# Kernel tuning notes

Hardware: AMD Instinct MI355X
Metric: run time of the kernel (lower is better)

The kernel has to match this reference:

```python
import jax, jax.numpy as jnp
import numpy as np

EPS = 1e-5
NEG_SLOPE = 0.1


def setup_inputs() -> dict:
    key = jax.random.key(0)
    ks = jax.random.split(key, 4)
    B, Cin, Cout, D, E, EMB = 2, 32, 32, 40, 3, 1
    return {
        "x": jax.random.normal(ks[0], (B, Cin, D, D, D), dtype=jnp.float32),
        "embedding": jax.random.normal(ks[1], (B, EMB), dtype=jnp.float32),
        "route_w": jax.random.normal(ks[2], (EMB, E), dtype=jnp.float32),
        "route_b": jnp.zeros((E,), dtype=jnp.float32),
        "expert_kernels": jax.random.normal(ks[3], (E, Cout, Cin, 3, 3, 3), dtype=jnp.float32) * 0.05,
        "expert_bias": jnp.zeros((E, Cout), dtype=jnp.float32),
        "gamma": jnp.ones((Cout,), dtype=jnp.float32),
        "beta": jnp.zeros((Cout,), dtype=jnp.float32),
    }


def reference(x, embedding, route_w, route_b, expert_kernels, expert_bias, gamma, beta):
    # CondConv routing: sigmoid(Linear(embedding)) -> per-sample expert weights [B, E]
    r = jax.nn.sigmoid(embedding @ route_w + route_b)
    # Per-sample combined kernel [B, O, I, 3, 3, 3] and bias [B, O]
    w = jnp.einsum('be,eoixyz->boixyz', r, expert_kernels)
    b = r @ expert_bias

    def conv_one(xi, wi):
        # xi: [Cin, D, H, W], wi: [O, I, 3, 3, 3] -> [Cout, D, H, W]
        return jax.lax.conv_general_dilated(
            xi[None], wi, window_strides=(1, 1, 1), padding='SAME',
            dimension_numbers=('NCDHW', 'OIDHW', 'NCDHW'))[0]

    y = jax.vmap(conv_one)(x, w) + b[:, :, None, None, None]  # [B, O, D, H, W]

    # BatchNorm3d (training mode: biased batch stats over B,D,H,W per channel)
    mean = jnp.mean(y, axis=(0, 2, 3, 4), keepdims=True)
    var = jnp.mean(jnp.square(y - mean), axis=(0, 2, 3, 4), keepdims=True)
    y = (y - mean) * jax.lax.rsqrt(var + EPS)
    y = y * gamma[None, :, None, None, None] + beta[None, :, None, None, None]

    # LeakyReLU(0.1)
    y = jnp.where(y >= 0, y, NEG_SLOPE * y)

    # Upsample nearest, scale_factor=2 on all 3 spatial dims
    y = jnp.repeat(jnp.repeat(jnp.repeat(y, 2, axis=2), 2, axis=3), 2, axis=4)
    return y
```

## Files before the change

kernel.cpp:

```cpp
#include <hip/hip_runtime.h>
#include <hip/hip_bf16.h>
#include <math.h>

#define BB   2
#define CIN  32
#define COUT 32
#define DM   40
#define PD   42
#define NPTS (DM*DM)
#define NVOL (DM*DM*DM)
#define EPSBN 1e-5f
#define NSLOT 64

typedef short  bf16x8  __attribute__((ext_vector_type(8)));
typedef short  bf16x4  __attribute__((ext_vector_type(4)));
typedef float  floatx4 __attribute__((ext_vector_type(4)));

#define WS_WFRAG 0
#define WS_BCOMB 27648
#define WS_SUM2  27712
#define WS_XPAD2 31808
#define WS_Y     2402624

#define REPACK_BLOCKS (PD*PD*BB)
#define NW_ELEMS  (2*2*27*64*8)
#define PREP_ELEMS (NW_ELEMS + 64 + NSLOT*64)
#define PREP_BLOCKS ((PREP_ELEMS + 255) / 256)

static __device__ __forceinline__ short f2bf(float f) {
    __hip_bfloat16 h = __float2bfloat16(f);
    return *reinterpret_cast<short*>(&h);
}
static __device__ __forceinline__ float bf2f(short s) {
    union { unsigned u; float f; } cv;
    cv.u = ((unsigned)(unsigned short)s) << 16;
    return cv.f;
}

__global__ void prep_repack_kernel(const float* __restrict__ x,
                                   const float* __restrict__ emb,
                                   const float* __restrict__ rw,
                                   const float* __restrict__ rb,
                                   const float* __restrict__ ek,
                                   const float* __restrict__ ebias,
                                   float* __restrict__ ws) {
    __shared__ __hip_bfloat16 tile[PD * 32];
    const int bid = blockIdx.x;
    const int t = threadIdx.x;
    if (bid < REPACK_BLOCKS) {
        int b  = bid / (PD * PD);
        int r  = bid % (PD * PD);
        int zp = r / PD, yp = r % PD;
        __hip_bfloat16* row = (__hip_bfloat16*)(ws + WS_XPAD2) +
                              ((((size_t)b * PD + zp) * PD + yp) * PD) * 32;
        const bool inz = (zp >= 1 && zp <= DM && yp >= 1 && yp <= DM);
        const int i  = t >> 3;
        const int xl = t & 7;
        #pragma unroll
        for (int k = 0; k < 6; ++k) {
            int xp = xl + 8 * k;
            if (xp < PD) {
                float v = 0.0f;
                if (inz && xp >= 1 && xp <= DM)
                    v = x[(size_t)(b * CIN + i) * NVOL +
                          (zp - 1) * NPTS + (yp - 1) * DM + (xp - 1)];
                tile[xp * 32 + i] = __float2bfloat16(v);
            }
        }
        __syncthreads();
        const unsigned* ts = (const unsigned*)tile;
        unsigned* rowu = (unsigned*)row;
        for (int j = t; j < PD * 32 / 2; j += 256) rowu[j] = ts[j];
        return;
    }
    int idx = (bid - REPACK_BLOCKS) * 256 + t;
    __hip_bfloat16* wfrag = (__hip_bfloat16*)(ws + WS_WFRAG);
    if (idx < NW_ELEMS) {
        int j    = idx & 7;
        int lane = (idx >> 3) & 63;
        int tap  = (idx >> 9) % 27;
        int nt   = (idx / (27 * 512)) & 1;
        int b    = idx / (2 * 27 * 512);
        int o = nt * 16 + (lane & 15);
        int i = (lane >> 4) * 8 + j;
        float e0 = emb[b];
        float w = 0.0f;
        #pragma unroll
        for (int e = 0; e < 3; ++e) {
            float r = 1.0f / (1.0f + expf(-(e0 * rw[e] + rb[e])));
            w += r * ek[((e * COUT + o) * CIN + i) * 27 + tap];
        }
        wfrag[idx] = __float2bfloat16(w);
    } else if (idx < NW_ELEMS + 64) {
        int j2 = idx - NW_ELEMS;
        int b = j2 >> 5, o = j2 & 31;
        float e0 = emb[b];
        float bv = 0.0f;
        #pragma unroll
        for (int e = 0; e < 3; ++e) {
            float r = 1.0f / (1.0f + expf(-(e0 * rw[e] + rb[e])));
            bv += r * ebias[e * COUT + o];
        }
        ws[WS_BCOMB + j2] = bv;
    } else if (idx < PREP_ELEMS) {
        ws[WS_SUM2 + (idx - NW_ELEMS - 64)] = 0.0f;
    }
}

__global__ __launch_bounds__(256, 8) void conv_mfma_kernel(
        const __hip_bfloat16* __restrict__ xp2,
        const bf16x8* __restrict__ wfrag,
        const float* __restrict__ bcomb,
        __hip_bfloat16* __restrict__ y,
        float* __restrict__ sums2) {
    const int g   = blockIdx.x & 7;
    const int s   = blockIdx.x >> 3;
    const int b   = s / 125;
    const int rem = s % 125;
    const int z   = g * 5 + rem / 25;
    const int mc  = rem % 25;

    const int tid = threadIdx.x, lane = tid & 63, wv = tid >> 6;
    const int mt = wv & 1, nt = wv >> 1;
    const int quad = lane >> 4, l15 = lane & 15;

    __shared__ float lstat[64];
    __shared__ short ytile[32 * 72];

    if (tid < 64) lstat[tid] = 0.0f;
    __syncthreads();

    const int pa0 = mc * 64 + mt * 32 + l15;
    const int pa1 = pa0 + 16;
    const int ya0 = pa0 / DM, xa0 = pa0 % DM;
    const int ya1 = pa1 / DM, xa1 = pa1 % DM;
    const char* abase0 = (const char*)xp2 +
        ((((size_t)b * PD + z) * PD + ya0) * PD + xa0) * 64 + quad * 16;
    const char* abase1 = (const char*)xp2 +
        ((((size_t)b * PD + z) * PD + ya1) * PD + xa1) * 64 + quad * 16;
    const bf16x8* wbase = wfrag + ((b * 2 + nt) * 27) * 64 + lane;

    floatx4 acc0 = {0.f, 0.f, 0.f, 0.f};
    floatx4 acc1 = {0.f, 0.f, 0.f, 0.f};
    #pragma unroll
    for (int t = 0; t < 27; ++t) {
        const int dz = t / 9, dy = (t / 3) % 3, dx = t % 3;
        const int aoff = ((dz * PD + dy) * PD + dx) * 64;
        bf16x8 av0 = *(const bf16x8*)(abase0 + aoff);
        bf16x8 av1 = *(const bf16x8*)(abase1 + aoff);
        bf16x8 bv  = wbase[t * 64];
        acc0 = __builtin_amdgcn_mfma_f32_16x16x32_bf16(av0, bv, acc0, 0, 0, 0);
        acc1 = __builtin_amdgcn_mfma_f32_16x16x32_bf16(av1, bv, acc1, 0, 0, 0);
    }

    const int o = nt * 16 + l15;
    const float bias = bcomb[b * COUT + o];

    float u0 = acc0[0] + bias, u1 = acc0[1] + bias;
    float u2 = acc0[2] + bias, u3 = acc0[3] + bias;
    float w0 = acc1[0] + bias, w1 = acc1[1] + bias;
    float w2 = acc1[2] + bias, w3 = acc1[3] + bias;

    {
        const int s0 = mt * 32 + quad * 4;
        bf16x4 p0 = { f2bf(u0), f2bf(u1), f2bf(u2), f2bf(u3) };
        bf16x4 p1 = { f2bf(w0), f2bf(w1), f2bf(w2), f2bf(w3) };
        *(bf16x4*)&ytile[o * 72 + s0]      = p0;
        *(bf16x4*)&ytile[o * 72 + s0 + 16] = p1;
    }

    float vs = u0 + u1 + u2 + u3 + w0 + w1 + w2 + w3;
    float vq = u0*u0 + u1*u1 + u2*u2 + u3*u3 + w0*w0 + w1*w1 + w2*w2 + w3*w3;
    vs += __shfl_xor(vs, 16); vq += __shfl_xor(vq, 16);
    vs += __shfl_xor(vs, 32); vq += __shfl_xor(vq, 32);
    if (lane < 16) {
        atomicAdd(&lstat[o],      vs);
        atomicAdd(&lstat[32 + o], vq);
    }
    __syncthreads();

    {
        const int o2 = tid >> 3, c = tid & 7;
        bf16x8 v = *(const bf16x8*)&ytile[o2 * 72 + c * 8];
        __hip_bfloat16* dst = y + ((size_t)(b * COUT + o2) * DM + z) * NPTS
                            + mc * 64 + c * 8;
        *(bf16x8*)dst = v;
    }
    if (tid < 64) {
        int slot = ((b * DM + z) * 25 + mc) & (NSLOT - 1);
        atomicAdd(&sums2[slot * 64 + tid], lstat[tid]);
    }
}

__global__ __launch_bounds__(256) void upsample_kernel(
        const __hip_bfloat16* __restrict__ yin,
        const float* __restrict__ sums2,
        const float* __restrict__ gamma,
        const float* __restrict__ beta,
        float* __restrict__ out) {
    __shared__ float partl[4][64];
    __shared__ float ssc[32], ssh[32];
    __shared__ float fplane[NPTS];
    const int tid = threadIdx.x;
    const int cc  = blockIdx.x / DM;
    const int z   = blockIdx.x % DM;
    const int c   = cc & 31;

    {
        int sg = tid >> 6, st = tid & 63;
        float p = 0.0f;
        #pragma unroll
        for (int s = 0; s < 16; ++s) p += sums2[(sg * 16 + s) * 64 + st];
        partl[sg][st] = p;
    }
    __syncthreads();
    if (tid < 64) {
        partl[0][tid] += partl[1][tid] + partl[2][tid] + partl[3][tid];
    }
    __syncthreads();
    if (tid < 32) {
        const float invN = 1.0f / (float)(BB * NVOL);
        float mean  = partl[0][tid] * invN;
        float var   = partl[0][32 + tid] * invN - mean * mean;
        float scale = gamma[tid] * rsqrtf(var + EPSBN);
        ssc[tid] = scale;
        ssh[tid] = beta[tid] - mean * scale;
    }
    __syncthreads();

    const float sc = ssc[c], sh = ssh[c];
    if (tid < NPTS / 8) {
        bf16x8 rv = *(const bf16x8*)(yin + ((size_t)cc * DM + z) * NPTS + tid * 8);
        #pragma unroll
        for (int j = 0; j < 8; ++j) {
            float v = bf2f(rv[j]) * sc + sh;
            fplane[tid * 8 + j] = (v >= 0.0f) ? v : 0.1f * v;
        }
    }
    __syncthreads();

    float* outp = out + ((size_t)cc * 80 + 2 * z) * 6400;
    #pragma unroll 2
    for (int cch = tid; cch < 2 * 1600; cch += 256) {
        int plane = cch / 1600;
        int cp    = cch - plane * 1600;
        int yy2   = cp / 20;
        int sx0   = (cp % 20) * 2;
        const float* srow = fplane + (yy2 >> 1) * DM;
        float v0 = srow[sx0], v1 = srow[sx0 + 1];
        floatx4 q = {v0, v0, v1, v1};
        *(floatx4*)(outp + (size_t)plane * 6400 + cp * 4) = q;
    }
}

extern "C" void kernel_launch(void* const* d_in, const int* in_sizes, int n_in,
                              void* d_out, int out_size, void* d_ws, size_t ws_size,
                              hipStream_t stream) {
    const float* x     = (const float*)d_in[0];
    const float* emb   = (const float*)d_in[1];
    const float* rw    = (const float*)d_in[2];
    const float* rb    = (const float*)d_in[3];
    const float* ek    = (const float*)d_in[4];
    const float* ebias = (const float*)d_in[5];
    const float* gamma = (const float*)d_in[6];
    const float* beta  = (const float*)d_in[7];
    float* ws  = (float*)d_ws;
    float* out = (float*)d_out;

    prep_repack_kernel<<<REPACK_BLOCKS + PREP_BLOCKS, 256, 0, stream>>>(
        x, emb, rw, rb, ek, ebias, ws);

    conv_mfma_kernel<<<2000, 256, 0, stream>>>(
        (const __hip_bfloat16*)(ws + WS_XPAD2), (const bf16x8*)(ws + WS_WFRAG),
        ws + WS_BCOMB, (__hip_bfloat16*)(ws + WS_Y), ws + WS_SUM2);

    upsample_kernel<<<BB * COUT * DM, 256, 0, stream>>>(
        (const __hip_bfloat16*)(ws + WS_Y), ws + WS_SUM2, gamma, beta, out);
}
```

Measured before the change: 198.3 us.

## Stage padded input rows in shared memory per depth slice for conv

The conv kernel now cooperatively copies the 5 padded input rows needed for each dz slice into LDS, then reads the 9 in-plane taps from shared memory instead of issuing direct global loads per tap. This cuts redundant global/L2 traffic across overlapping 3x3 windows. In exchange it adds two block barriers per dz, about 13 KB of extra LDS, and a load phase that is not overlapped with the MFMA work.

```diff
diff --git a/kernel.cpp b/kernel.cpp
--- a/kernel.cpp
+++ b/kernel.cpp
@@ -126,31 +126,44 @@
 
     __shared__ float lstat[64];
     __shared__ short ytile[32 * 72];
+    __shared__ short atile[5 * PD * 32];
 
     if (tid < 64) lstat[tid] = 0.0f;
-    __syncthreads();
-
+
+    const int y0  = (mc * 64) / DM;
     const int pa0 = mc * 64 + mt * 32 + l15;
     const int pa1 = pa0 + 16;
     const int ya0 = pa0 / DM, xa0 = pa0 % DM;
     const int ya1 = pa1 / DM, xa1 = pa1 % DM;
-    const char* abase0 = (const char*)xp2 +
-        ((((size_t)b * PD + z) * PD + ya0) * PD + xa0) * 64 + quad * 16;
-    const char* abase1 = (const char*)xp2 +
-        ((((size_t)b * PD + z) * PD + ya1) * PD + xa1) * 64 + quad * 16;
+    const int af0 = ((ya0 - y0) * PD + xa0) * 32 + quad * 8;
+    const int af1 = ((ya1 - y0) * PD + xa1) * 32 + quad * 8;
+
     const bf16x8* wbase = wfrag + ((b * 2 + nt) * 27) * 64 + lane;
+    const int nrows = min(5, PD - y0);
+    const int nchunk = nrows * (PD * 32 / 8);
 
     floatx4 acc0 = {0.f, 0.f, 0.f, 0.f};
     floatx4 acc1 = {0.f, 0.f, 0.f, 0.f};
-    #pragma unroll
-    for (int t = 0; t < 27; ++t) {
-        const int dz = t / 9, dy = (t / 3) % 3, dx = t % 3;
-        const int aoff = ((dz * PD + dy) * PD + dx) * 64;
-        bf16x8 av0 = *(const bf16x8*)(abase0 + aoff);
-        bf16x8 av1 = *(const bf16x8*)(abase1 + aoff);
-        bf16x8 bv  = wbase[t * 64];
-        acc0 = __builtin_amdgcn_mfma_f32_16x16x32_bf16(av0, bv, acc0, 0, 0, 0);
-        acc1 = __builtin_amdgcn_mfma_f32_16x16x32_bf16(av1, bv, acc1, 0, 0, 0);
+
+    for (int dz = 0; dz < 3; ++dz) {
+        __syncthreads();
+        {
+            const bf16x8* src = (const bf16x8*)(xp2 +
+                ((((size_t)b * PD + (z + dz)) * PD + y0) * PD) * 32);
+            bf16x8* dst = (bf16x8*)atile;
+            for (int j = tid; j < nchunk; j += 256) dst[j] = src[j];
+        }
+        __syncthreads();
+        #pragma unroll
+        for (int t9 = 0; t9 < 9; ++t9) {
+            const int dy = t9 / 3, dx = t9 % 3;
+            const int aoff = (dy * PD + dx) * 32;
+            bf16x8 av0 = *(const bf16x8*)&atile[af0 + aoff];
+            bf16x8 av1 = *(const bf16x8*)&atile[af1 + aoff];
+            bf16x8 bv  = wbase[(dz * 9 + t9) * 64];
+            acc0 = __builtin_amdgcn_mfma_f32_16x16x32_bf16(av0, bv, acc0, 0, 0, 0);
+            acc1 = __builtin_amdgcn_mfma_f32_16x16x32_bf16(av1, bv, acc1, 0, 0, 0);
+        }
     }
 
     const int o = nt * 16 + l15;
```

Result: faster. 179.5 us, median of 2 (-9.5%).
